# Optimization experiments

Hardware: AMD Instinct MI355X
Metric: run time of the kernel (lower is better)

Reference implementation:

```python
import jax, jax.numpy as jnp
import numpy as np

NORM_EPS = 1e-6
QK_SCALE = 1.0 / 128.0  # 1/d_head (muP)
ROTARY_BASE = 10000
INFTY_APPROX = 1e30

B, T, M, H, D = 2, 2048, 1024, 8, 128


def _rmsnorm(x, eps=NORM_EPS):
    # normalize over the last (head) dim; no learned gains (norm_gains=False)
    ms = jnp.mean(jnp.square(x), axis=-1, keepdims=True)
    return x / jnp.sqrt(ms + eps)


def _rope(x, base=ROTARY_BASE):
    # x: [b, h, t, d]; rotate (even-half, odd-half) pairs as in the source
    length, width = x.shape[-2], x.shape[-1]
    half = width // 2
    pos = jnp.arange(length, dtype=x.dtype)[:, None]            # [t, 1]
    freqs = jnp.power(jnp.asarray(base, x.dtype), -jnp.arange(half, dtype=x.dtype) / half)[None, :]
    rad = pos * freqs                                            # [t, half]
    cos = jnp.cos(rad)[None, None]
    sin = jnp.sin(rad)[None, None]
    even, odd = jnp.split(x, 2, axis=-1)
    return jnp.concatenate([even * cos - odd * sin, even * sin + odd * cos], axis=-1)


def setup_inputs() -> dict:
    key = jax.random.key(0)
    ks = jax.random.split(key, 5)
    std = M ** -0.5
    return {
        "x": jax.random.normal(ks[0], (B, T, M), jnp.float32),
        "wq": jax.random.normal(ks[1], (M, H, D), jnp.float32) * std,
        "wk": jax.random.normal(ks[2], (M, H, D), jnp.float32) * std,
        "wv": jax.random.normal(ks[3], (M, H, D), jnp.float32) * std,
        "wo": jax.random.normal(ks[4], (H, D, M), jnp.float32) * std,
    }


def reference(x, wq, wk, wv, wo):
    # projections: [b, h, t, d]
    q = jnp.einsum('bim,mhd->bhid', x, wq)
    k = jnp.einsum('bim,mhd->bhid', x, wk)
    v = jnp.einsum('bim,mhd->bhid', x, wv)
    # qk RMSNorm (norm_gains=False)
    q = _rmsnorm(q)
    k = _rmsnorm(k)
    # inline RoPE
    q = _rope(q)
    k = _rope(k)
    # scaled scores: mult applied to both q and k (mult^2 = qk_scale)
    mult = jnp.asarray(QK_SCALE ** 0.5, q.dtype)
    s = jnp.einsum('bhid,bhjd->bhij', q * mult, k * mult)
    # causal mask: subtract large constant where i < j
    t = s.shape[-1]
    mask = (jnp.arange(t)[:, None] < jnp.arange(t)[None, :]).astype(s.dtype)
    s = s - jnp.asarray(INFTY_APPROX, s.dtype) * mask[None, None]
    p = jax.nn.softmax(s, axis=-1)
    o = jnp.einsum('bhij,bhjd->bhid', p, v)
    return jnp.einsum('bhid,hdm->bim', o, wo)
```

## Files before the change

### kernel.cpp

```cpp
#include <hip/hip_runtime.h>
#include <hip/hip_bf16.h>
#include <math.h>

#define B_  2
#define T_  2048
#define M_  1024
#define H_  8
#define D_  128
#define NROW (B_ * T_)
#define HD  (H_ * D_)

#define NORM_EPS 1e-6f
#define QK_MULT  0.08838834764831845f
#define LN_BASE_64 0.14391156510f

typedef short bf16x8  __attribute__((ext_vector_type(8)));
typedef float f32x4   __attribute__((ext_vector_type(4)));
typedef float f32x16  __attribute__((ext_vector_type(16)));

static __device__ __forceinline__ unsigned short f2bf(float f) {
    union { __hip_bfloat16 h; unsigned short u; } cv;
    cv.h = __float2bfloat16(f);
    return cv.u;
}
static __device__ __forceinline__ float bf2f(unsigned short u) {
    union { unsigned short u; __hip_bfloat16 h; } cv;
    cv.u = u;
    return __bfloat162float(cv.h);
}
static __device__ __forceinline__ unsigned int pk2bf(float a, float b) {
    return ((unsigned int)f2bf(b) << 16) | f2bf(a);
}

static __device__ __forceinline__ void gload_lds16(const unsigned short* g,
                                                   unsigned short* l) {
    __builtin_amdgcn_global_load_lds(
        (const __attribute__((address_space(1))) void*)g,
        (__attribute__((address_space(3))) void*)l, 16, 0, 0);
}

__global__ __launch_bounds__(256) void prep(const float* __restrict__ x,
                                            const float* __restrict__ w0,
                                            const float* __restrict__ w1,
                                            const float* __restrict__ w2,
                                            const float* __restrict__ w3,
                                            unsigned short* __restrict__ xb,
                                            unsigned short* __restrict__ wqkvT,
                                            unsigned short* __restrict__ woT)
{
    __shared__ float t[32][33];
    const int z = blockIdx.z;
    if (z == 4) {
        const size_t base = ((size_t)blockIdx.y * 32 + blockIdx.x) * 4096;
        #pragma unroll
        for (int it = 0; it < 4; ++it) {
            const size_t i = base + it * 1024 + threadIdx.x * 4;
            const float4 v = *(const float4*)(x + i);
            ushort4 o;
            o.x = f2bf(v.x); o.y = f2bf(v.y); o.z = f2bf(v.z); o.w = f2bf(v.w);
            *(ushort4*)(xb + i) = o;
        }
        return;
    }
    const float* in = z == 0 ? w0 : (z == 1 ? w1 : (z == 2 ? w2 : w3));
    unsigned short* out = z < 3 ? (wqkvT + (size_t)z * 1024 * 1024) : woT;

    const int tx = threadIdx.x & 31;
    const int ty = threadIdx.x >> 5;
    const int n0 = blockIdx.x * 32;
    const int k0 = blockIdx.y * 32;
    #pragma unroll
    for (int r = 0; r < 4; ++r)
        t[ty + r * 8][tx] = in[(size_t)(k0 + ty + r * 8) * 1024 + n0 + tx];
    __syncthreads();
    #pragma unroll
    for (int r = 0; r < 4; ++r)
        out[(size_t)(n0 + ty + r * 8) * 1024 + k0 + tx] = f2bf(t[tx][ty + r * 8]);
}

__global__ __launch_bounds__(256) void gemm_qkv(const unsigned short* __restrict__ A,
                                                const unsigned short* __restrict__ Bt,
                                                unsigned short* __restrict__ oq,
                                                unsigned short* __restrict__ ok,
                                                unsigned short* __restrict__ vt)
{
    __shared__ unsigned short As[2][128 * 64];
    __shared__ unsigned short Bs[2][128 * 64];

    const int tid  = threadIdx.x;
    const int lane = tid & 63;
    const int w    = tid >> 6;
    const int g    = lane >> 4;
    const int lc   = lane & 15;

    const int m0 = blockIdx.y * 128;
    const int n0 = blockIdx.x * 128;

    const unsigned short* aBase = A  + (size_t)m0 * 1024;
    const unsigned short* bBase = Bt + (size_t)n0 * 1024;

    int dstOff[4];
    size_t srcOff[4];
    #pragma unroll
    for (int it = 0; it < 4; ++it) {
        const int u  = tid + it * 256;
        const int r2 = u >> 3;
        const int sg = (u & 7) ^ (r2 & 7);
        dstOff[it] = u * 8;
        srcOff[it] = (size_t)r2 * 1024 + sg * 8;
    }

    f32x4 acc[2][8];
    #pragma unroll
    for (int i = 0; i < 2; ++i)
        #pragma unroll
        for (int j = 0; j < 8; ++j)
            acc[i][j] = (f32x4){0.f, 0.f, 0.f, 0.f};

    #pragma unroll
    for (int it = 0; it < 4; ++it) {
        gload_lds16(aBase + srcOff[it], &As[0][dstOff[it]]);
        gload_lds16(bBase + srcOff[it], &Bs[0][dstOff[it]]);
    }

    for (int kt = 0; kt < 16; ++kt) {
        const int cur = kt & 1;
        __syncthreads();

        if (kt < 15) {
            const int k0n = (kt + 1) * 64;
            #pragma unroll
            for (int it = 0; it < 4; ++it) {
                gload_lds16(aBase + srcOff[it] + k0n, &As[cur ^ 1][dstOff[it]]);
                gload_lds16(bBase + srcOff[it] + k0n, &Bs[cur ^ 1][dstOff[it]]);
            }
        }

        #pragma unroll
        for (int dc = 0; dc < 2; ++dc) {
            const int sw = ((dc * 4 + g) ^ (lc & 7)) << 3;
            bf16x8 af[2], bfr[8];
            #pragma unroll
            for (int i = 0; i < 2; ++i)
                af[i] = *(const bf16x8*)&As[cur][(w * 32 + i * 16 + lc) * 64 + sw];
            #pragma unroll
            for (int j = 0; j < 8; ++j)
                bfr[j] = *(const bf16x8*)&Bs[cur][(j * 16 + lc) * 64 + sw];

            #pragma unroll
            for (int i = 0; i < 2; ++i)
                #pragma unroll
                for (int j = 0; j < 8; ++j)
                    acc[i][j] = __builtin_amdgcn_mfma_f32_16x16x32_bf16(af[i], bfr[j], acc[i][j], 0, 0, 0);
        }
    }

    const int which = n0 >> 10;
    const int ncol0 = n0 & 1023;
    if (which < 2) {
        unsigned short* outp = which == 0 ? oq : ok;
        float freq[4];
        #pragma unroll
        for (int j = 0; j < 4; ++j)
            freq[j] = __expf(-(float)(j * 16 + lc) * LN_BASE_64);

        #pragma unroll
        for (int i = 0; i < 2; ++i)
            #pragma unroll
            for (int r = 0; r < 4; ++r) {
                float s = 0.f;
                #pragma unroll
                for (int j = 0; j < 8; ++j) s += acc[i][j][r] * acc[i][j][r];
                #pragma unroll
                for (int off = 1; off < 16; off <<= 1) s += __shfl_xor(s, off);
                const float rms = rsqrtf(s * (1.0f / 128.0f) + NORM_EPS) * QK_MULT;

                const int trow = m0 + w * 32 + i * 16 + g * 4 + r;
                const float tpos = (float)(trow & (T_ - 1));
                unsigned short* op = outp + (size_t)trow * 1024 + ncol0;
                #pragma unroll
                for (int j = 0; j < 4; ++j) {
                    float sn, cs;
                    __sincosf(tpos * freq[j], &sn, &cs);
                    const float e = acc[i][j][r] * rms;
                    const float o = acc[i][j + 4][r] * rms;
                    op[j * 16 + lc]      = f2bf(e * cs - o * sn);
                    op[j * 16 + lc + 64] = f2bf(e * sn + o * cs);
                }
            }
    } else {
        const int b2 = m0 >> 11;
        const int hh = ncol0 >> 7;
        #pragma unroll
        for (int i = 0; i < 2; ++i) {
            const int t = (m0 & 2047) + w * 32 + i * 16 + g * 4;
            #pragma unroll
            for (int j = 0; j < 8; ++j) {
                const int dd = j * 16 + lc;
                uint2 val;
                val.x = pk2bf(acc[i][j][0], acc[i][j][1]);
                val.y = pk2bf(acc[i][j][2], acc[i][j][3]);
                *(uint2*)(vt + (((size_t)(b2 * 8 + hh) * 128 + dd) * T_ + t)) = val;
            }
        }
    }
}

__global__ __launch_bounds__(256) void gemm_out(const unsigned short* __restrict__ A,
                                                const unsigned short* __restrict__ Bt,
                                                float* __restrict__ cf)
{
    __shared__ unsigned short As[2][128 * 64];
    __shared__ unsigned short Bs[2][64 * 64];

    const int tid  = threadIdx.x;
    const int lane = tid & 63;
    const int w    = tid >> 6;
    const int g    = lane >> 4;
    const int lc   = lane & 15;
    const int wm   = w >> 1;
    const int wn   = w & 1;

    const int m0 = blockIdx.y * 128;
    const int n0 = blockIdx.x * 64;

    const unsigned short* aBase = A  + (size_t)m0 * 1024;
    const unsigned short* bBase = Bt + (size_t)n0 * 1024;

    int dstA[4], dstB[2];
    size_t srcA[4], srcB[2];
    #pragma unroll
    for (int it = 0; it < 4; ++it) {
        const int u  = tid + it * 256;
        const int r2 = u >> 3;
        const int sg = (u & 7) ^ (r2 & 7);
        dstA[it] = u * 8;
        srcA[it] = (size_t)r2 * 1024 + sg * 8;
    }
    #pragma unroll
    for (int it = 0; it < 2; ++it) {
        const int u  = tid + it * 256;
        const int r2 = u >> 3;
        const int sg = (u & 7) ^ (r2 & 7);
        dstB[it] = u * 8;
        srcB[it] = (size_t)r2 * 1024 + sg * 8;
    }

    f32x4 acc[4][2];
    #pragma unroll
    for (int i = 0; i < 4; ++i)
        #pragma unroll
        for (int j = 0; j < 2; ++j)
            acc[i][j] = (f32x4){0.f, 0.f, 0.f, 0.f};

    #pragma unroll
    for (int it = 0; it < 4; ++it)
        gload_lds16(aBase + srcA[it], &As[0][dstA[it]]);
    #pragma unroll
    for (int it = 0; it < 2; ++it)
        gload_lds16(bBase + srcB[it], &Bs[0][dstB[it]]);

    for (int kt = 0; kt < 16; ++kt) {
        const int cur = kt & 1;
        __syncthreads();

        if (kt < 15) {
            const int k0n = (kt + 1) * 64;
            #pragma unroll
            for (int it = 0; it < 4; ++it)
                gload_lds16(aBase + srcA[it] + k0n, &As[cur ^ 1][dstA[it]]);
            #pragma unroll
            for (int it = 0; it < 2; ++it)
                gload_lds16(bBase + srcB[it] + k0n, &Bs[cur ^ 1][dstB[it]]);
        }

        #pragma unroll
        for (int dc = 0; dc < 2; ++dc) {
            const int sw = ((dc * 4 + g) ^ (lc & 7)) << 3;
            bf16x8 af[4], bfr[2];
            #pragma unroll
            for (int i = 0; i < 4; ++i)
                af[i] = *(const bf16x8*)&As[cur][(wm * 64 + i * 16 + lc) * 64 + sw];
            #pragma unroll
            for (int j = 0; j < 2; ++j)
                bfr[j] = *(const bf16x8*)&Bs[cur][(wn * 32 + j * 16 + lc) * 64 + sw];

            #pragma unroll
            for (int i = 0; i < 4; ++i)
                #pragma unroll
                for (int j = 0; j < 2; ++j)
                    acc[i][j] = __builtin_amdgcn_mfma_f32_16x16x32_bf16(af[i], bfr[j], acc[i][j], 0, 0, 0);
        }
    }

    #pragma unroll
    for (int i = 0; i < 4; ++i) {
        const int mrow = m0 + wm * 64 + i * 16 + g * 4;
        #pragma unroll
        for (int j = 0; j < 2; ++j) {
            const int nc = n0 + wn * 32 + j * 16 + lc;
            #pragma unroll
            for (int r = 0; r < 4; ++r)
                cf[(size_t)(mrow + r) * 1024 + nc] = acc[i][j][r];
        }
    }
}

__global__ __launch_bounds__(256) void flash_attn(const unsigned short* __restrict__ qb,
                                                  const unsigned short* __restrict__ kb,
                                                  const unsigned short* __restrict__ vt,
                                                  unsigned short* __restrict__ o)
{
    __shared__ __align__(16) unsigned short smem[2 * 64 * 128 + 2 * 128 * 64 + 128];
    unsigned short* KsB = smem;
    unsigned short* VsB = smem + 2 * 64 * 128;
    float* lscr = (float*)(smem + 2 * 64 * 128 + 2 * 128 * 64);
    float* scr  = (float*)smem;

    const int tid  = threadIdx.x;
    const int lane = tid & 63;
    const int w    = tid >> 6;
    const int wj   = w >> 1;
    const int wq2  = w & 1;
    const int qcol = lane & 31;
    const int hi   = lane >> 5;

    const int bh = blockIdx.x;
    const int h  = bh & (H_ - 1);
    const int b  = bh >> 3;
    const int yy = blockIdx.y;
    const int qt = (yy & 1) ? (31 - (yy >> 1)) : (yy >> 1);
    const int q0 = qt * 64;

    const size_t bhbase  = (size_t)b * T_ * HD + (size_t)h * 128;
    const size_t bhvbase = (size_t)bh * 128 * T_;

    int mI[4];
    size_t srcKoff[4], srcVoff[4];
    #pragma unroll
    for (int it = 0; it < 4; ++it) {
        const int m = (w * 4 + it) * 64 + lane;
        mI[it] = m;
        const int jK = m >> 4, cK = (m & 15) ^ (jK & 15);
        srcKoff[it] = (size_t)jK * 1024 + cK * 8;
        const int dV = m >> 3, cV = (m & 7) ^ (dV & 7);
        srcVoff[it] = (size_t)dV * T_ + cV * 8;
    }
    const unsigned short* kgb = kb + bhbase;
    const unsigned short* vgb = vt + bhvbase;

    bf16x8 qf[8];
    {
        const unsigned short* qp = qb + bhbase + (size_t)(q0 + wq2 * 32 + qcol) * 1024 + hi * 8;
        #pragma unroll
        for (int ks = 0; ks < 8; ++ks)
            qf[ks] = *(const bf16x8*)(qp + ks * 16);
    }

    float lsum = 0.f;
    f32x16 otacc[4];
    #pragma unroll
    for (int dch = 0; dch < 4; ++dch)
        #pragma unroll
        for (int r = 0; r < 16; ++r) otacc[dch][r] = 0.f;

    #pragma unroll
    for (int it = 0; it < 4; ++it) {
        gload_lds16(kgb + srcKoff[it], &KsB[mI[it] * 8]);
        gload_lds16(vgb + srcVoff[it], &VsB[mI[it] * 8]);
    }

    for (int jt = 0; jt <= qt; ++jt) {
        const int cur = jt & 1;
        unsigned short* Ks = KsB + cur * (64 * 128);
        unsigned short* Vs = VsB + cur * (128 * 64);
        __syncthreads();

        if (jt < qt) {
            const size_t j0n = (size_t)(jt + 1) * 64;
            unsigned short* Kn = KsB + (cur ^ 1) * (64 * 128);
            unsigned short* Vn = VsB + (cur ^ 1) * (128 * 64);
            #pragma unroll
            for (int it = 0; it < 4; ++it) {
                gload_lds16(kgb + j0n * 1024 + srcKoff[it], &Kn[mI[it] * 8]);
                gload_lds16(vgb + j0n + srcVoff[it], &Vn[mI[it] * 8]);
            }
        }

        const bool dead = (jt == qt) && (wj > wq2);
        if (!dead) {
            f32x16 sacc;
            #pragma unroll
            for (int r = 0; r < 16; ++r) sacc[r] = 0.f;
            const int jrow = wj * 32 + qcol;
            #pragma unroll
            for (int ks = 0; ks < 8; ++ks) {
                const int c = ks * 2 + hi;
                bf16x8 af = *(const bf16x8*)&Ks[(jrow * 16 + (c ^ (lane & 15))) * 8];
                sacc = __builtin_amdgcn_mfma_f32_32x32x16_bf16(af, qf[ks], sacc, 0, 0, 0);
            }

            if (jt == qt && wj == wq2) {
                #pragma unroll
                for (int r = 0; r < 16; ++r) {
                    const int jl = (r & 3) + 8 * (r >> 2) + 4 * hi;
                    if (qcol < jl) sacc[r] = -1e30f;
                }
            }

            unsigned int dw[8];
            #pragma unroll
            for (int m2 = 0; m2 < 8; ++m2) {
                const float p0 = __expf(sacc[2 * m2]);
                const float p1 = __expf(sacc[2 * m2 + 1]);
                lsum += p0 + p1;
                dw[m2] = pk2bf(p0, p1);
            }
            unsigned int ex[8];
            #pragma unroll
            for (int m2 = 0; m2 < 8; ++m2)
                ex[m2] = (unsigned int)__shfl_xor((int)dw[m2], 32);

            #pragma unroll
            for (int ks2 = 0; ks2 < 2; ++ks2) {
                union { unsigned int u[4]; bf16x8 v; } pf;
                pf.u[0] = hi ? ex[4 * ks2 + 2] : dw[4 * ks2 + 0];
                pf.u[1] = hi ? ex[4 * ks2 + 3] : dw[4 * ks2 + 1];
                pf.u[2] = hi ? dw[4 * ks2 + 2] : ex[4 * ks2 + 0];
                pf.u[3] = hi ? dw[4 * ks2 + 3] : ex[4 * ks2 + 1];
                #pragma unroll
                for (int dch = 0; dch < 4; ++dch) {
                    const int c = wj * 4 + ks2 * 2 + hi;
                    const int drow = dch * 32 + qcol;
                    bf16x8 af = *(const bf16x8*)&Vs[(drow * 8 + (c ^ (lane & 7))) * 8];
                    otacc[dch] = __builtin_amdgcn_mfma_f32_32x32x16_bf16(af, pf.v, otacc[dch], 0, 0, 0);
                }
            }
        }
    }

    lsum += __shfl_xor(lsum, 32);
    __syncthreads();

    if (wj == 1) {
        float* s0 = scr + (size_t)(wq2 * 32 + qcol) * 129;
        #pragma unroll
        for (int dch = 0; dch < 4; ++dch)
            #pragma unroll
            for (int r = 0; r < 16; ++r)
                s0[dch * 32 + (r & 3) + 8 * (r >> 2) + 4 * hi] = otacc[dch][r];
        if (hi == 0) lscr[wq2 * 32 + qcol] = lsum;
    }
    __syncthreads();
    if (wj == 0) {
        const float l = lsum + lscr[wq2 * 32 + qcol];
        const float inv = 1.0f / l;
        const float* s0 = scr + (size_t)(wq2 * 32 + qcol) * 129;
        unsigned short* op = o + bhbase + (size_t)(q0 + wq2 * 32 + qcol) * 1024;
        #pragma unroll
        for (int dch = 0; dch < 4; ++dch) {
            #pragma unroll
            for (int k4 = 0; k4 < 4; ++k4) {
                const int d0 = dch * 32 + 8 * k4 + 4 * hi;
                const float f0 = (otacc[dch][4 * k4 + 0] + s0[d0 + 0]) * inv;
                const float f1 = (otacc[dch][4 * k4 + 1] + s0[d0 + 1]) * inv;
                const float f2 = (otacc[dch][4 * k4 + 2] + s0[d0 + 2]) * inv;
                const float f3 = (otacc[dch][4 * k4 + 3] + s0[d0 + 3]) * inv;
                uint2 val;
                val.x = pk2bf(f0, f1);
                val.y = pk2bf(f2, f3);
                *(uint2*)(op + d0) = val;
            }
        }
    }
}

extern "C" void kernel_launch(void* const* d_in, const int* in_sizes, int n_in,
                              void* d_out, int out_size, void* d_ws, size_t ws_size,
                              hipStream_t stream)
{
    const float* x  = (const float*)d_in[0];
    const float* wq = (const float*)d_in[1];
    const float* wk = (const float*)d_in[2];
    const float* wv = (const float*)d_in[3];
    const float* wo = (const float*)d_in[4];
    float* out = (float*)d_out;

    const size_t SZ = (size_t)NROW * HD;
    unsigned short* qb    = (unsigned short*)d_ws;
    unsigned short* kb    = qb + SZ;
    unsigned short* vt    = kb + SZ;
    unsigned short* ob    = vt + SZ;
    unsigned short* xb    = ob + SZ;
    unsigned short* wqkvT = xb + SZ;
    unsigned short* woT   = wqkvT + 3 * 1024 * 1024;

    prep<<<dim3(32, 32, 5), 256, 0, stream>>>(x, wq, wk, wv, wo, xb, wqkvT, woT);

    gemm_qkv<<<dim3(24, 32), 256, 0, stream>>>(xb, wqkvT, qb, kb, vt);

    flash_attn<<<dim3(B_ * H_, 32), 256, 0, stream>>>(qb, kb, vt, ob);

    gemm_out<<<dim3(16, 32), 256, 0, stream>>>(ob, woT, out);
}
```

Baseline: 187.1 us.

## Shrink QKV GEMM k-tile, split QK accumulator chains, use permlane32 swap in attention

The QKV GEMM now uses a 32-wide k-tile with half-size double-buffered LDS and 32 iterations, aiming for more occupancy at the cost of more barriers. In attention, the QK^T MFMA chain is split into two independent accumulators to shorten dependency stalls, and the shuffle-based P exchange is replaced with permlane32_swap. The change also adds s_setprio around the MFMA sections and switches the causal tile ordering to a fold-over mapping. The new tile ordering changes load balance, and the extra barriers and the vector add could offset some of the intended gains.

```diff
diff --git a/kernel.cpp b/kernel.cpp
--- a/kernel.cpp
+++ b/kernel.cpp
@@ -17,6 +17,7 @@
 typedef short bf16x8  __attribute__((ext_vector_type(8)));
 typedef float f32x4   __attribute__((ext_vector_type(4)));
 typedef float f32x16  __attribute__((ext_vector_type(16)));
+typedef unsigned int uint32x2 __attribute__((ext_vector_type(2)));
 
 static __device__ __forceinline__ unsigned short f2bf(float f) {
     union { __hip_bfloat16 h; unsigned short u; } cv;
@@ -84,8 +85,8 @@
                                                 unsigned short* __restrict__ ok,
                                                 unsigned short* __restrict__ vt)
 {
-    __shared__ unsigned short As[2][128 * 64];
-    __shared__ unsigned short Bs[2][128 * 64];
+    __shared__ unsigned short As[2][128 * 32];
+    __shared__ unsigned short Bs[2][128 * 32];
 
     const int tid  = threadIdx.x;
     const int lane = tid & 63;
@@ -99,13 +100,13 @@
     const unsigned short* aBase = A  + (size_t)m0 * 1024;
     const unsigned short* bBase = Bt + (size_t)n0 * 1024;
 
-    int dstOff[4];
-    size_t srcOff[4];
-    #pragma unroll
-    for (int it = 0; it < 4; ++it) {
+    int dstOff[2];
+    size_t srcOff[2];
+    #pragma unroll
+    for (int it = 0; it < 2; ++it) {
         const int u  = tid + it * 256;
-        const int r2 = u >> 3;
-        const int sg = (u & 7) ^ (r2 & 7);
+        const int r2 = u >> 2;
+        const int sg = (u & 3) ^ (r2 & 3);
         dstOff[it] = u * 8;
         srcOff[it] = (size_t)r2 * 1024 + sg * 8;
     }
@@ -118,41 +119,38 @@
             acc[i][j] = (f32x4){0.f, 0.f, 0.f, 0.f};
 
     #pragma unroll
-    for (int it = 0; it < 4; ++it) {
+    for (int it = 0; it < 2; ++it) {
         gload_lds16(aBase + srcOff[it], &As[0][dstOff[it]]);
         gload_lds16(bBase + srcOff[it], &Bs[0][dstOff[it]]);
     }
 
-    for (int kt = 0; kt < 16; ++kt) {
+    for (int kt = 0; kt < 32; ++kt) {
         const int cur = kt & 1;
         __syncthreads();
 
-        if (kt < 15) {
-            const int k0n = (kt + 1) * 64;
-            #pragma unroll
-            for (int it = 0; it < 4; ++it) {
+        if (kt < 31) {
+            const int k0n = (kt + 1) * 32;
+            #pragma unroll
+            for (int it = 0; it < 2; ++it) {
                 gload_lds16(aBase + srcOff[it] + k0n, &As[cur ^ 1][dstOff[it]]);
                 gload_lds16(bBase + srcOff[it] + k0n, &Bs[cur ^ 1][dstOff[it]]);
             }
         }
 
-        #pragma unroll
-        for (int dc = 0; dc < 2; ++dc) {
-            const int sw = ((dc * 4 + g) ^ (lc & 7)) << 3;
-            bf16x8 af[2], bfr[8];
-            #pragma unroll
-            for (int i = 0; i < 2; ++i)
-                af[i] = *(const bf16x8*)&As[cur][(w * 32 + i * 16 + lc) * 64 + sw];
+        const int sw = (g ^ (lc & 3)) << 3;
+        bf16x8 af[2], bfr[8];
+        #pragma unroll
+        for (int i = 0; i < 2; ++i)
+            af[i] = *(const bf16x8*)&As[cur][(w * 32 + i * 16 + lc) * 32 + sw];
+        #pragma unroll
+        for (int j = 0; j < 8; ++j)
+            bfr[j] = *(const bf16x8*)&Bs[cur][(j * 16 + lc) * 32 + sw];
+
+        #pragma unroll
+        for (int i = 0; i < 2; ++i)
             #pragma unroll
             for (int j = 0; j < 8; ++j)
-                bfr[j] = *(const bf16x8*)&Bs[cur][(j * 16 + lc) * 64 + sw];
-
-            #pragma unroll
-            for (int i = 0; i < 2; ++i)
-                #pragma unroll
-                for (int j = 0; j < 8; ++j)
-                    acc[i][j] = __builtin_amdgcn_mfma_f32_16x16x32_bf16(af[i], bfr[j], acc[i][j], 0, 0, 0);
-        }
+                acc[i][j] = __builtin_amdgcn_mfma_f32_16x16x32_bf16(af[i], bfr[j], acc[i][j], 0, 0, 0);
     }
 
     const int which = n0 >> 10;
@@ -329,7 +327,7 @@
     const int h  = bh & (H_ - 1);
     const int b  = bh >> 3;
     const int yy = blockIdx.y;
-    const int qt = (yy & 1) ? (31 - (yy >> 1)) : (yy >> 1);
+    const int qt = yy < 16 ? yy : 47 - yy;
     const int q0 = qt * 64;
 
     const size_t bhbase  = (size_t)b * T_ * HD + (size_t)h * 128;
@@ -389,16 +387,22 @@
 
         const bool dead = (jt == qt) && (wj > wq2);
         if (!dead) {
-            f32x16 sacc;
-            #pragma unroll
-            for (int r = 0; r < 16; ++r) sacc[r] = 0.f;
+            f32x16 sacc0, sacc1;
+            #pragma unroll
+            for (int r = 0; r < 16; ++r) { sacc0[r] = 0.f; sacc1[r] = 0.f; }
             const int jrow = wj * 32 + qcol;
-            #pragma unroll
-            for (int ks = 0; ks < 8; ++ks) {
-                const int c = ks * 2 + hi;
-                bf16x8 af = *(const bf16x8*)&Ks[(jrow * 16 + (c ^ (lane & 15))) * 8];
-                sacc = __builtin_amdgcn_mfma_f32_32x32x16_bf16(af, qf[ks], sacc, 0, 0, 0);
-            }
+            __builtin_amdgcn_s_setprio(1);
+            #pragma unroll
+            for (int ks = 0; ks < 8; ks += 2) {
+                const int c0 = ks * 2 + hi;
+                bf16x8 af0 = *(const bf16x8*)&Ks[(jrow * 16 + (c0 ^ (lane & 15))) * 8];
+                sacc0 = __builtin_amdgcn_mfma_f32_32x32x16_bf16(af0, qf[ks], sacc0, 0, 0, 0);
+                const int c1 = (ks + 1) * 2 + hi;
+                bf16x8 af1 = *(const bf16x8*)&Ks[(jrow * 16 + (c1 ^ (lane & 15))) * 8];
+                sacc1 = __builtin_amdgcn_mfma_f32_32x32x16_bf16(af1, qf[ks + 1], sacc1, 0, 0, 0);
+            }
+            __builtin_amdgcn_s_setprio(0);
+            f32x16 sacc = sacc0 + sacc1;
 
             if (jt == qt && wj == wq2) {
                 #pragma unroll
@@ -416,18 +420,19 @@
                 lsum += p0 + p1;
                 dw[m2] = pk2bf(p0, p1);
             }
-            unsigned int ex[8];
-            #pragma unroll
-            for (int m2 = 0; m2 < 8; ++m2)
-                ex[m2] = (unsigned int)__shfl_xor((int)dw[m2], 32);
 
             #pragma unroll
             for (int ks2 = 0; ks2 < 2; ++ks2) {
+                const uint32x2 s02 = __builtin_amdgcn_permlane32_swap(
+                    dw[4 * ks2 + 0], dw[4 * ks2 + 2], 0, 0);
+                const uint32x2 s13 = __builtin_amdgcn_permlane32_swap(
+                    dw[4 * ks2 + 1], dw[4 * ks2 + 3], 0, 0);
                 union { unsigned int u[4]; bf16x8 v; } pf;
-                pf.u[0] = hi ? ex[4 * ks2 + 2] : dw[4 * ks2 + 0];
-                pf.u[1] = hi ? ex[4 * ks2 + 3] : dw[4 * ks2 + 1];
-                pf.u[2] = hi ? dw[4 * ks2 + 2] : ex[4 * ks2 + 0];
-                pf.u[3] = hi ? dw[4 * ks2 + 3] : ex[4 * ks2 + 1];
+                pf.u[0] = s02[0];
+                pf.u[1] = s13[0];
+                pf.u[2] = s02[1];
+                pf.u[3] = s13[1];
+                __builtin_amdgcn_s_setprio(1);
                 #pragma unroll
                 for (int dch = 0; dch < 4; ++dch) {
                     const int c = wj * 4 + ks2 * 2 + hi;
@@ -435,6 +440,7 @@
                     bf16x8 af = *(const bf16x8*)&Vs[(drow * 8 + (c ^ (lane & 7))) * 8];
                     otacc[dch] = __builtin_amdgcn_mfma_f32_32x32x16_bf16(af, pf.v, otacc[dch], 0, 0, 0);
                 }
+                __builtin_amdgcn_s_setprio(0);
             }
         }
     }
```

Result: faster. 180.1 us (-3.8%).
